# Kernel optimization log

Hardware: AMD Instinct MI355X
Metric: run time of the kernel (lower is better)

## Reference

```python
import jax, jax.numpy as jnp
import numpy as np

N_BITS = 8
Q_LEVELS = N_BITS ** 2 - 1  # note: original uses n_bits**2 - 1, not 2**n_bits - 1
GRID_RES = (128, 512, 2048)  # 2**7, 2**9, 2**11
BITWIDTH = 6
CODE_SIZE = 4


def _qround(x, axis):
    mn = jnp.min(x, axis=axis, keepdims=True)
    mx = jnp.max(x, axis=axis, keepdims=True)
    scale = jnp.maximum(mx - mn, 1e-8) / Q_LEVELS
    return jnp.round((x - mn) / scale) * scale + mn


def _ste(q, x):
    # straight-through estimator: forward q, gradient of x
    return jax.lax.stop_gradient(q - x) + x


def _qalinear(x, w, b):
    w_q = _ste(_qround(w, (-2, -1)), w)
    b_q = _ste(_qround(b, -1), b)
    return x @ w_q + b_q


def _grid(coords, indices, codebook, res):
    # coords: [N] in [-1, 1]; indices: [res, 2**bitwidth]; codebook: [2**bitwidth, code_size]
    soft_grid = jax.nn.softmax(indices, axis=-1) @ codebook           # [res, C]
    max_grid = codebook[jnp.argmax(indices, axis=1)]                  # [res, C]
    grid = _ste(max_grid, soft_grid)
    c = (coords + 1.0) / 2.0 * (res - 1)
    left = jnp.minimum(jnp.floor(c), res - 2).astype(jnp.int32)
    right = jnp.maximum(jnp.ceil(c), 1).astype(jnp.int32)
    w = (c - left)[..., None]                                         # [N, 1]
    return (1.0 - w) * grid[left] + w * grid[right]                   # [N, C]


def setup_inputs() -> dict:
    key = jax.random.key(0)
    ks = jax.random.split(key, 20)
    N = 1 << 20
    x_coord = jax.random.uniform(ks[0], (N, 1), jnp.float32, -1.0, 1.0)
    x_feat = jax.random.uniform(ks[1], (N, 1), jnp.float32, -1.0, 1.0)
    x = jnp.concatenate([x_feat, x_coord], axis=-1)  # last dim is the grid coordinate
    inp = {"x": x}
    for gi, res in enumerate(GRID_RES):
        inp[f"cb{gi}"] = 0.01 * jax.random.normal(ks[2 + 2 * gi], (2 ** BITWIDTH, CODE_SIZE), jnp.float32)
        inp[f"ind{gi}"] = 0.01 * jax.random.normal(ks[3 + 2 * gi], (res, 2 ** BITWIDTH), jnp.float32)
    dims = [(5, 64), (64, 64), (64, 64), (64, 64), (64, 1)]
    for li, (di, do) in enumerate(dims):
        inp[f"w{li}"] = (2 * jax.random.uniform(ks[8 + 2 * li], (di, do), jnp.float32) - 1) / np.sqrt(di)
        inp[f"b{li}"] = (2 * jax.random.uniform(ks[9 + 2 * li], (do,), jnp.float32) - 1) / np.sqrt(di)
    return inp


def reference(x, cb0, ind0, cb1, ind1, cb2, ind2,
              w0, b0, w1, b1, w2, b2, w3, b3, w4, b4):
    coords = x[..., -1]
    g = (_grid(coords, ind0, cb0, GRID_RES[0])
         + _grid(coords, ind1, cb1, GRID_RES[1])
         + _grid(coords, ind2, cb2, GRID_RES[2]))           # [N, 4]
    h = jnp.concatenate([g, x[..., :-1]], axis=-1)          # [N, 5]
    h = _qalinear(h, w0, b0)
    for w, b in ((w1, b1), (w2, b2), (w3, b3)):
        h = _qalinear(jax.nn.gelu(h, approximate=False), w, b)
    h = _qalinear(jax.nn.gelu(h, approximate=False), w4, b4)
    return jnp.tanh(h)
```

## Files before the change

kernel.cpp:

```cpp
#include <hip/hip_runtime.h>
#include <hip/hip_bf16.h>
#include <math.h>

#define BQ0 320
#define BQ1 4480
#define BQ2 8640
#define BQ3 12800
#define BQ4 12928
#define GT0 12932
#define GT1 13444
#define GT2 15492
#define FRAG_OFF 23684
#define W4P 38020
#define WSCALE 64.0f
#define WINV   0.015625f

typedef _Float16 f16x8 __attribute__((ext_vector_type(8)));
typedef _Float16 f16x2 __attribute__((ext_vector_type(2)));
typedef float floatx4 __attribute__((ext_vector_type(4)));
typedef float floatx2 __attribute__((ext_vector_type(2)));
typedef unsigned int uintx4 __attribute__((ext_vector_type(4)));

__device__ inline floatx4 mfma16(f16x8 a, f16x8 b, floatx4 c) {
    return __builtin_amdgcn_mfma_f32_16x16x32_f16(a, b, c, 0, 0, 0);
}
__device__ inline floatx2 splat2(float c) { return (floatx2){c, c}; }

__device__ inline unsigned int pkrtz(float a, float b) {
    auto r = __builtin_amdgcn_cvt_pkrtz(a, b);
    return __builtin_bit_cast(unsigned int, r);
}
__device__ inline unsigned int pack_f16(float a, float b) {
    unsigned short ua = __builtin_bit_cast(unsigned short, (_Float16)a);
    unsigned short ub = __builtin_bit_cast(unsigned short, (_Float16)b);
    return (unsigned int)ua | ((unsigned int)ub << 16);
}
__device__ inline f16x8 frag_from(uint2 a, uint2 b) {
    uintx4 u = {a.x, a.y, b.x, b.y};
    return __builtin_bit_cast(f16x8, u);
}
__device__ inline f16x2 h2(unsigned int u) { return __builtin_bit_cast(f16x2, u); }

#if __has_builtin(__builtin_amdgcn_fdot2)
__device__ inline float fdot2f(f16x2 a, f16x2 b, float c) {
    return __builtin_amdgcn_fdot2(a, b, c, false);
}
#else
__device__ inline float fdot2f(f16x2 a, f16x2 b, float c) {
    return fmaf((float)a[0], (float)b[0], fmaf((float)a[1], (float)b[1], c));
}
#endif

__device__ inline floatx2 gelu2(floatx2 x) {
    floatx2 ax = __builtin_elementwise_abs(x);
    floatx2 z  = ax * splat2(0.70710678118654752f);
    floatx2 den = __builtin_elementwise_fma(z, splat2(0.47047f), splat2(1.0f));
    floatx2 t;
    t.x = __builtin_amdgcn_rcpf(den.x);
    t.y = __builtin_amdgcn_rcpf(den.y);
    floatx2 p = __builtin_elementwise_fma(t, splat2(0.7478556f), splat2(-0.0958798f));
    p = __builtin_elementwise_fma(t, p, splat2(0.3480242f));
    p = p * t;
    floatx2 ea = (z * z) * splat2(-1.44269504088896f);
    floatx2 e;
    e.x = __builtin_amdgcn_exp2f(ea.x);
    e.y = __builtin_amdgcn_exp2f(ea.y);
    floatx2 er = __builtin_elementwise_fma(-p, e, splat2(1.0f));
    return __builtin_elementwise_fma(ax, er, x) * splat2(0.5f);
}

__device__ inline float tanh_fast(float x) {
    float e = __builtin_amdgcn_exp2f(x * 2.88539008177793f);
    return fmaf(-2.0f, __builtin_amdgcn_rcpf(e + 1.0f), 1.0f);
}

__device__ void block_minmax(float mn, float mx, float* omn, float* omx,
                             float* smn, float* smx) {
    __syncthreads();
    #pragma unroll
    for (int off = 32; off > 0; off >>= 1) {
        mn = fminf(mn, __shfl_down(mn, off));
        mx = fmaxf(mx, __shfl_down(mx, off));
    }
    int wid = threadIdx.x >> 6, lane = threadIdx.x & 63;
    if (lane == 0) { smn[wid] = mn; smx[wid] = mx; }
    __syncthreads();
    if (threadIdx.x == 0) {
        float a = smn[0], b = smx[0];
        for (int i = 1; i < 4; ++i) { a = fminf(a, smn[i]); b = fmaxf(b, smx[i]); }
        smn[0] = a; smx[0] = b;
    }
    __syncthreads();
    *omn = smn[0]; *omx = smx[0];
}

__device__ void quantize_tensor(const float* __restrict__ src, int n,
                                float* __restrict__ dst, float* smn, float* smx) {
    float mn = 3.4e38f, mx = -3.4e38f;
    for (int i = threadIdx.x; i < n; i += blockDim.x) {
        float v = src[i];
        mn = fminf(mn, v); mx = fmaxf(mx, v);
    }
    float gmn, gmx;
    block_minmax(mn, mx, &gmn, &gmx, smn, smx);
    float scale = fmaxf(gmx - gmn, 1e-8f) / 63.0f;
    for (int i = threadIdx.x; i < n; i += blockDim.x) {
        float v = src[i];
        dst[i] = rintf((v - gmn) / scale) * scale + gmn;
    }
}

__global__ void vinr_prep(
    const float* __restrict__ cb0, const float* __restrict__ ind0,
    const float* __restrict__ cb1, const float* __restrict__ ind1,
    const float* __restrict__ cb2, const float* __restrict__ ind2,
    const float* __restrict__ w0, const float* __restrict__ b0,
    const float* __restrict__ w1, const float* __restrict__ b1,
    const float* __restrict__ w2, const float* __restrict__ b2,
    const float* __restrict__ w3, const float* __restrict__ b3,
    const float* __restrict__ w4, const float* __restrict__ b4,
    float* __restrict__ ws)
{
    __shared__ float smn[4], smx[4];
    if (blockIdx.x < 5) {
        switch (blockIdx.x) {
            case 0: quantize_tensor(b0, 64, ws + BQ0, smn, smx); break;
            case 1: quantize_tensor(b1, 64, ws + BQ1, smn, smx); break;
            case 2: quantize_tensor(b2, 64, ws + BQ2, smn, smx); break;
            case 3: quantize_tensor(b3, 64, ws + BQ3, smn, smx); break;
            case 4: quantize_tensor(b4, 1,  ws + BQ4, smn, smx); break;
        }
    } else if (blockIdx.x < 16) {
        int r = (int)(blockIdx.x - 5) * 256 + (int)threadIdx.x;
        const float* ind = nullptr; const float* cb = nullptr; float* dst = nullptr;
        if (r < 128)       { ind = ind0 + r * 64;          cb = cb0; dst = ws + GT0 + r * 4; }
        else if (r < 640)  { int rr = r - 128;  ind = ind1 + rr * 64; cb = cb1; dst = ws + GT1 + rr * 4; }
        else if (r < 2688) { int rr = r - 640;  ind = ind2 + rr * 64; cb = cb2; dst = ws + GT2 + rr * 4; }
        if (dst) {
            float best = -3.4e38f; int bi = 0;
            for (int j = 0; j < 64; ++j) {
                float v = ind[j];
                if (v > best) { best = v; bi = j; }
            }
            #pragma unroll
            for (int d = 0; d < 4; ++d) dst[d] = cb[bi * 4 + d];
        }
    } else if (blockIdx.x < 40) {
        if (threadIdx.x < 64) {
            int fi = (int)blockIdx.x - 16;
            int lane = (int)threadIdx.x;
            int l = fi >> 3, s = (fi >> 2) & 1, ft = fi & 3;
            const float* w = (l == 0) ? w1 : (l == 1) ? w2 : w3;
            float mn = 3.4e38f, mx = -3.4e38f;
            for (int i = lane; i < 4096; i += 64) {
                float v = w[i];
                mn = fminf(mn, v); mx = fmaxf(mx, v);
            }
            #pragma unroll
            for (int off = 32; off > 0; off >>= 1) {
                mn = fminf(mn, __shfl_xor(mn, off));
                mx = fmaxf(mx, __shfl_xor(mx, off));
            }
            float scale = fmaxf(mx - mn, 1e-8f) / 63.0f;
            int q = lane >> 4, m15 = lane & 15;
            int n = ft * 16 + m15;
            f16x8 hi;
            #pragma unroll
            for (int j = 0; j < 8; ++j) {
                int k = s * 32 + (j >> 2) * 16 + q * 4 + (j & 3);
                float v = w[k * 64 + n];
                v = (rintf((v - mn) / scale) * scale + mn) * WSCALE;
                hi[j] = (_Float16)v;
            }
            f16x8* base = (f16x8*)(ws + FRAG_OFF);
            base[fi * 64 + lane] = hi;
        }
    } else if (blockIdx.x == 40) {
        int wv = (int)threadIdx.x >> 6;
        int lane = (int)threadIdx.x & 63;
        if (wv < 4) {
            float mn = 3.4e38f, mx = -3.4e38f;
            for (int i = lane; i < 320; i += 64) {
                float v = w0[i];
                mn = fminf(mn, v); mx = fmaxf(mx, v);
            }
            #pragma unroll
            for (int off = 32; off > 0; off >>= 1) {
                mn = fminf(mn, __shfl_xor(mn, off));
                mx = fmaxf(mx, __shfl_xor(mx, off));
            }
            float scale = fmaxf(mx - mn, 1e-8f) / 63.0f;
            int q = lane >> 4, m15 = lane & 15;
            int n = wv * 16 + m15;
            f16x8 hi;
            #pragma unroll
            for (int j = 0; j < 8; ++j) {
                int k = q * 8 + j;
                float v = 0.0f;
                if (k < 5) {
                    float vv = w0[k * 64 + n];
                    v = (rintf((vv - mn) / scale) * scale + mn) * WSCALE;
                }
                hi[j] = (_Float16)v;
            }
            f16x8* base = (f16x8*)(ws + FRAG_OFF);
            base[(24 + wv) * 64 + lane] = hi;
        }
    } else {
        if (threadIdx.x < 64) {
            int lane = (int)threadIdx.x;
            float v = w4[lane];
            float mn = v, mx = v;
            #pragma unroll
            for (int off = 32; off > 0; off >>= 1) {
                mn = fminf(mn, __shfl_xor(mn, off));
                mx = fmaxf(mx, __shfl_xor(mx, off));
            }
            float scale = fmaxf(mx - mn, 1e-8f) / 63.0f;
            if (lane < 32) {
                int t0 = 2 * lane, t1 = t0 + 1;
                int f0 = ((t0 >> 5) * 32) + (((t0 >> 2) & 1) * 16)
                       + (((t0 >> 3) & 3) * 4) + (t0 & 3);
                int f1 = ((t1 >> 5) * 32) + (((t1 >> 2) & 1) * 16)
                       + (((t1 >> 3) & 3) * 4) + (t1 & 3);
                float q0 = (rintf((w4[f0] - mn) / scale) * scale + mn) * WSCALE;
                float q1 = (rintf((w4[f1] - mn) / scale) * scale + mn) * WSCALE;
                unsigned int* wsU = (unsigned int*)ws;
                wsU[W4P + lane] = pack_f16(q0, q1);
            }
        }
    }
}

__global__ __launch_bounds__(256, 4) void vinr_main(
    const float* __restrict__ x, const float* __restrict__ ws,
    float* __restrict__ out, int N)
{
    __shared__ __align__(16) uint4 ilds[4][32];
    int wave = threadIdx.x >> 6, lane = threadIdx.x & 63;
    int q = lane >> 4, m15 = lane & 15;
    int p = lane & 31, half = lane >> 5;

    int base = (int)blockIdx.x * 128 + wave * 32;
    int idx = base + p;
    int idxc = min(idx, N - 1);
    float2 xr = ((const float2*)x)[idxc];
    float feat  = xr.x;
    float coord = xr.y;

    float g0 = 0.f, g1 = 0.f, g2 = 0.f, g3 = 0.f;
    const int RES[3]  = {128, 512, 2048};
    const int GOFF[3] = {GT0, GT1, GT2};
    #pragma unroll
    for (int gi = 0; gi < 3; ++gi) {
        int res = RES[gi];
        float c = (coord + 1.0f) * 0.5f * (float)(res - 1);
        int left  = min((int)floorf(c), res - 2);
        int right = max((int)ceilf(c), 1);
        float w = c - (float)left;
        const float4* gt = (const float4*)(ws + GOFF[gi]);
        float4 gl = gt[left];
        float4 gr = gt[right];
        float wm = 1.0f - w;
        g0 += wm * gl.x + w * gr.x;
        g1 += wm * gl.y + w * gr.y;
        g2 += wm * gl.z + w * gr.z;
        g3 += wm * gl.w + w * gr.w;
    }

    if (half == 0)
        ilds[wave][p] = make_uint4(pack_f16(g0, g1), pack_f16(g2, g3),
                                   pack_f16(feat, 0.0f), 0u);

    const f16x8* fh = (const f16x8*)(ws + FRAG_OFF);
    f16x8 zfrag = __builtin_bit_cast(f16x8, (uintx4){0u, 0u, 0u, 0u});

    f16x8 Bc[2][2];
    floatx4 acc[4][2];
    const int BOFF[4] = {BQ0, BQ1, BQ2, BQ3};

    #pragma unroll
    for (int l = 0; l < 4; ++l) {
        #pragma unroll
        for (int ft = 0; ft < 4; ++ft)
            #pragma unroll
            for (int pt = 0; pt < 2; ++pt)
                acc[ft][pt] = (floatx4){0.f, 0.f, 0.f, 0.f};

        if (l == 0) {
            f16x8 B0[2];
            #pragma unroll
            for (int pt = 0; pt < 2; ++pt) {
                B0[pt] = zfrag;
                if (q == 0) {
                    uint4 r = ilds[wave][pt * 16 + m15];
                    B0[pt] = frag_from(make_uint2(r.x, r.y), make_uint2(r.z, r.w));
                }
            }
            #pragma unroll
            for (int ft = 0; ft < 4; ++ft) {
                f16x8 Wh = fh[(24 + ft) * 64 + lane];
                #pragma unroll
                for (int pt = 0; pt < 2; ++pt)
                    acc[ft][pt] = mfma16(Wh, B0[pt], acc[ft][pt]);
            }
        } else {
            #pragma unroll
            for (int s = 0; s < 2; ++s) {
                #pragma unroll
                for (int ft = 0; ft < 4; ++ft) {
                    f16x8 Wh = fh[(((l - 1) * 2 + s) * 4 + ft) * 64 + lane];
                    #pragma unroll
                    for (int pt = 0; pt < 2; ++pt)
                        acc[ft][pt] = mfma16(Wh, Bc[s][pt], acc[ft][pt]);
                }
            }
        }

        int bb = BOFF[l];
        #pragma unroll
        for (int sh = 0; sh < 2; ++sh) {
            float4 bA = *(const float4*)(ws + bb + (2 * sh)     * 16 + q * 4);
            float4 bB = *(const float4*)(ws + bb + (2 * sh + 1) * 16 + q * 4);
            #pragma unroll
            for (int pt = 0; pt < 2; ++pt) {
                floatx4 a0 = acc[2 * sh][pt];
                floatx4 a1 = acc[2 * sh + 1][pt];
                floatx2 u01 = gelu2(__builtin_elementwise_fma(
                    (floatx2){a0[0], a0[1]}, splat2(WINV), (floatx2){bA.x, bA.y}));
                floatx2 u23 = gelu2(__builtin_elementwise_fma(
                    (floatx2){a0[2], a0[3]}, splat2(WINV), (floatx2){bA.z, bA.w}));
                floatx2 v01 = gelu2(__builtin_elementwise_fma(
                    (floatx2){a1[0], a1[1]}, splat2(WINV), (floatx2){bB.x, bB.y}));
                floatx2 v23 = gelu2(__builtin_elementwise_fma(
                    (floatx2){a1[2], a1[3]}, splat2(WINV), (floatx2){bB.z, bB.w}));
                uintx4 wv = {pkrtz(u01.x, u01.y), pkrtz(u23.x, u23.y),
                             pkrtz(v01.x, v01.y), pkrtz(v23.x, v23.y)};
                Bc[sh][pt] = __builtin_bit_cast(f16x8, wv);
            }
        }
    }

    {
        const unsigned int* wsU = (const unsigned int*)ws;
        float ah0 = 0.0f, ah1 = 0.0f;
        #pragma unroll
        for (int s = 0; s < 2; ++s) {
            uint4 wv = *(const uint4*)(wsU + W4P + 16 * s + 4 * q);
            uintx4 b0 = __builtin_bit_cast(uintx4, Bc[s][0]);
            uintx4 b1 = __builtin_bit_cast(uintx4, Bc[s][1]);
            ah0 = fdot2f(h2(b0[0]), h2(wv.x), ah0);
            ah1 = fdot2f(h2(b1[0]), h2(wv.x), ah1);
            ah0 = fdot2f(h2(b0[1]), h2(wv.y), ah0);
            ah1 = fdot2f(h2(b1[1]), h2(wv.y), ah1);
            ah0 = fdot2f(h2(b0[2]), h2(wv.z), ah0);
            ah1 = fdot2f(h2(b1[2]), h2(wv.z), ah1);
            ah0 = fdot2f(h2(b0[3]), h2(wv.w), ah0);
            ah1 = fdot2f(h2(b1[3]), h2(wv.w), ah1);
        }
        ah0 += __shfl_xor(ah0, 16);
        ah0 += __shfl_xor(ah0, 32);
        ah1 += __shfl_xor(ah1, 16);
        ah1 += __shfl_xor(ah1, 32);
        float b4v = ws[BQ4];
        int oidx = base + lane;
        if (lane < 32 && oidx < N) {
            float sel = (lane & 16) ? ah1 : ah0;
            out[oidx] = tanh_fast(fmaf(sel, WINV, b4v));
        }
    }
}

extern "C" void kernel_launch(void* const* d_in, const int* in_sizes, int n_in,
                              void* d_out, int out_size, void* d_ws, size_t ws_size,
                              hipStream_t stream) {
    const float* x    = (const float*)d_in[0];
    const float* cb0  = (const float*)d_in[1];
    const float* ind0 = (const float*)d_in[2];
    const float* cb1  = (const float*)d_in[3];
    const float* ind1 = (const float*)d_in[4];
    const float* cb2  = (const float*)d_in[5];
    const float* ind2 = (const float*)d_in[6];
    const float* w0 = (const float*)d_in[7],  * b0 = (const float*)d_in[8];
    const float* w1 = (const float*)d_in[9],  * b1 = (const float*)d_in[10];
    const float* w2 = (const float*)d_in[11], * b2 = (const float*)d_in[12];
    const float* w3 = (const float*)d_in[13], * b3 = (const float*)d_in[14];
    const float* w4 = (const float*)d_in[15], * b4 = (const float*)d_in[16];
    float* ws  = (float*)d_ws;
    float* out = (float*)d_out;

    int N = in_sizes[0] / 2;

    vinr_prep<<<42, 256, 0, stream>>>(cb0, ind0, cb1, ind1, cb2, ind2,
                                      w0, b0, w1, b1, w2, b2, w3, b3, w4, b4, ws);
    int blocks = (N + 127) / 128;
    vinr_main<<<blocks, 256, 0, stream>>>(x, ws, out, N);
}
```

Baseline: 211.4 us.

## Restructure MLP layers per output tile and raise occupancy bound to 6

Each hidden layer now computes one output feature tile at a time. It runs two chained MFMAs and applies bias and GELU right away, instead of keeping all eight accumulators live before the activation pass. This lowers live register pressure, and the launch bounds move from 4 to 6 blocks per SM to improve latency hiding. The risk is register spilling under the tighter bound, plus less MFMA/VALU overlap within a layer because each tile's GELU now depends directly on its MFMAs.

```diff
diff --git a/kernel.cpp b/kernel.cpp
--- a/kernel.cpp
+++ b/kernel.cpp
@@ -232,7 +232,7 @@
     }
 }
 
-__global__ __launch_bounds__(256, 4) void vinr_main(
+__global__ __launch_bounds__(256, 6) void vinr_main(
     const float* __restrict__ x, const float* __restrict__ ws,
     float* __restrict__ out, int N)
 {
@@ -274,71 +274,68 @@
 
     const f16x8* fh = (const f16x8*)(ws + FRAG_OFF);
     f16x8 zfrag = __builtin_bit_cast(f16x8, (uintx4){0u, 0u, 0u, 0u});
+    const floatx4 zacc = (floatx4){0.f, 0.f, 0.f, 0.f};
 
     f16x8 Bc[2][2];
-    floatx4 acc[4][2];
-    const int BOFF[4] = {BQ0, BQ1, BQ2, BQ3};
-
+    uintx4 Bn[2][2];
+
+    {
+        f16x8 B0[2];
+        #pragma unroll
+        for (int pt = 0; pt < 2; ++pt) {
+            B0[pt] = zfrag;
+            if (q == 0) {
+                uint4 r = ilds[wave][pt * 16 + m15];
+                B0[pt] = frag_from(make_uint2(r.x, r.y), make_uint2(r.z, r.w));
+            }
+        }
+        #pragma unroll
+        for (int ft = 0; ft < 4; ++ft) {
+            f16x8 Wh = fh[(24 + ft) * 64 + lane];
+            float4 bq = *(const float4*)(ws + BQ0 + ft * 16 + q * 4);
+            #pragma unroll
+            for (int pt = 0; pt < 2; ++pt) {
+                floatx4 av = mfma16(Wh, B0[pt], zacc);
+                floatx2 v01 = gelu2(__builtin_elementwise_fma(
+                    (floatx2){av[0], av[1]}, splat2(WINV), (floatx2){bq.x, bq.y}));
+                floatx2 v23 = gelu2(__builtin_elementwise_fma(
+                    (floatx2){av[2], av[3]}, splat2(WINV), (floatx2){bq.z, bq.w}));
+                Bn[ft >> 1][pt][(ft & 1) * 2]     = pkrtz(v01.x, v01.y);
+                Bn[ft >> 1][pt][(ft & 1) * 2 + 1] = pkrtz(v23.x, v23.y);
+            }
+        }
+        #pragma unroll
+        for (int s = 0; s < 2; ++s)
+            #pragma unroll
+            for (int pt = 0; pt < 2; ++pt)
+                Bc[s][pt] = __builtin_bit_cast(f16x8, Bn[s][pt]);
+    }
+
+    const int BOFF[3] = {BQ1, BQ2, BQ3};
     #pragma unroll
-    for (int l = 0; l < 4; ++l) {
-        #pragma unroll
-        for (int ft = 0; ft < 4; ++ft)
+    for (int l = 0; l < 3; ++l) {
+        #pragma unroll
+        for (int ft = 0; ft < 4; ++ft) {
+            f16x8 W0 = fh[(l * 8 + ft) * 64 + lane];
+            f16x8 W1 = fh[(l * 8 + 4 + ft) * 64 + lane];
+            float4 bq = *(const float4*)(ws + BOFF[l] + ft * 16 + q * 4);
+            #pragma unroll
+            for (int pt = 0; pt < 2; ++pt) {
+                floatx4 av = mfma16(W0, Bc[0][pt], zacc);
+                av = mfma16(W1, Bc[1][pt], av);
+                floatx2 v01 = gelu2(__builtin_elementwise_fma(
+                    (floatx2){av[0], av[1]}, splat2(WINV), (floatx2){bq.x, bq.y}));
+                floatx2 v23 = gelu2(__builtin_elementwise_fma(
+                    (floatx2){av[2], av[3]}, splat2(WINV), (floatx2){bq.z, bq.w}));
+                Bn[ft >> 1][pt][(ft & 1) * 2]     = pkrtz(v01.x, v01.y);
+                Bn[ft >> 1][pt][(ft & 1) * 2 + 1] = pkrtz(v23.x, v23.y);
+            }
+        }
+        #pragma unroll
+        for (int s = 0; s < 2; ++s)
             #pragma unroll
             for (int pt = 0; pt < 2; ++pt)
-                acc[ft][pt] = (floatx4){0.f, 0.f, 0.f, 0.f};
-
-        if (l == 0) {
-            f16x8 B0[2];
-            #pragma unroll
-            for (int pt = 0; pt < 2; ++pt) {
-                B0[pt] = zfrag;
-                if (q == 0) {
-                    uint4 r = ilds[wave][pt * 16 + m15];
-                    B0[pt] = frag_from(make_uint2(r.x, r.y), make_uint2(r.z, r.w));
-                }
-            }
-            #pragma unroll
-            for (int ft = 0; ft < 4; ++ft) {
-                f16x8 Wh = fh[(24 + ft) * 64 + lane];
-                #pragma unroll
-                for (int pt = 0; pt < 2; ++pt)
-                    acc[ft][pt] = mfma16(Wh, B0[pt], acc[ft][pt]);
-            }
-        } else {
-            #pragma unroll
-            for (int s = 0; s < 2; ++s) {
-                #pragma unroll
-                for (int ft = 0; ft < 4; ++ft) {
-                    f16x8 Wh = fh[(((l - 1) * 2 + s) * 4 + ft) * 64 + lane];
-                    #pragma unroll
-                    for (int pt = 0; pt < 2; ++pt)
-                        acc[ft][pt] = mfma16(Wh, Bc[s][pt], acc[ft][pt]);
-                }
-            }
-        }
-
-        int bb = BOFF[l];
-        #pragma unroll
-        for (int sh = 0; sh < 2; ++sh) {
-            float4 bA = *(const float4*)(ws + bb + (2 * sh)     * 16 + q * 4);
-            float4 bB = *(const float4*)(ws + bb + (2 * sh + 1) * 16 + q * 4);
-            #pragma unroll
-            for (int pt = 0; pt < 2; ++pt) {
-                floatx4 a0 = acc[2 * sh][pt];
-                floatx4 a1 = acc[2 * sh + 1][pt];
-                floatx2 u01 = gelu2(__builtin_elementwise_fma(
-                    (floatx2){a0[0], a0[1]}, splat2(WINV), (floatx2){bA.x, bA.y}));
-                floatx2 u23 = gelu2(__builtin_elementwise_fma(
-                    (floatx2){a0[2], a0[3]}, splat2(WINV), (floatx2){bA.z, bA.w}));
-                floatx2 v01 = gelu2(__builtin_elementwise_fma(
-                    (floatx2){a1[0], a1[1]}, splat2(WINV), (floatx2){bB.x, bB.y}));
-                floatx2 v23 = gelu2(__builtin_elementwise_fma(
-                    (floatx2){a1[2], a1[3]}, splat2(WINV), (floatx2){bB.z, bB.w}));
-                uintx4 wv = {pkrtz(u01.x, u01.y), pkrtz(u23.x, u23.y),
-                             pkrtz(v01.x, v01.y), pkrtz(v23.x, v23.y)};
-                Bc[sh][pt] = __builtin_bit_cast(f16x8, wv);
-            }
-        }
+                Bc[s][pt] = __builtin_bit_cast(f16x8, Bn[s][pt]);
     }
 
     {
```

Result: no change. 210.1 us (-0.6%).
